# Optimization experiments

Measured on AMD Instinct MI355X. Metric: run time of the kernel, lower is better.

The kernel has to match this reference:

```python
import jax, jax.numpy as jnp
import numpy as np

T, B, C, S = 4096, 8, 512, 2048


def setup_inputs() -> dict:
    key = jax.random.key(0)
    k1, k2, k3 = jax.random.split(key, 3)
    x = jax.random.normal(k1, (T, B, C), dtype=jnp.float32)
    downsampling_mask = jax.random.uniform(k2, (B, T, S), dtype=jnp.float32)
    size_of_groups = jax.random.randint(k3, (B, S), 0, 4, dtype=jnp.int64)
    leftmost_group = jnp.zeros((1, 1, C), dtype=jnp.float32)
    return {"x": x, "downsampling_mask": downsampling_mask,
            "size_of_groups": size_of_groups, "leftmost_group": leftmost_group}


def reference(x, downsampling_mask, size_of_groups, leftmost_group):
    # mode == 'average': masked grouped pooling as a dense contraction
    # x: [T,B,C], mask: [B,T,S] -> downsampled: [S,B,C]
    downsampled = jnp.einsum('tbc,bts->sbc', x, downsampling_mask)
    # prepend learned leftmost group embedding, broadcast over batch
    left = jnp.broadcast_to(leftmost_group, (1, x.shape[1], x.shape[2]))
    return jnp.concatenate([left, downsampled], axis=0)  # [S+1, B, C]
```

## Files before the change

### kernel.cpp

```cpp
#include <hip/hip_runtime.h>
#include <hip/hip_bf16.h>

constexpr int T  = 4096;
constexpr int Bb = 8;
constexpr int C  = 512;
constexpr int S  = 2048;
constexpr int BC = Bb * C;

constexpr int BK = 64;
constexpr int NK = T / BK;

typedef __bf16 bf16x8 __attribute__((ext_vector_type(8)));
typedef float  f32x16 __attribute__((ext_vector_type(16)));
typedef float  f32x4  __attribute__((ext_vector_type(4)));

__device__ inline unsigned pk2(float lo, float hi) {
    union { __hip_bfloat16 h; unsigned short u; } a, b;
    a.h = __float2bfloat16(lo);
    b.h = __float2bfloat16(hi);
    return ((unsigned)b.u << 16) | (unsigned)a.u;
}

__device__ inline int slot16(int s) { return s ^ ((s >> 2) & 7); }

__global__ void left_fill(const float* __restrict__ left, float* __restrict__ out) {
    int i = blockIdx.x * blockDim.x + threadIdx.x;
    if (i < BC) out[i] = left[i & (C - 1)];
}

__global__ __launch_bounds__(512, 4) void ds_gemm(
    const float* __restrict__ x,
    const float* __restrict__ mask,
    float* __restrict__ out)
{
    __shared__ __align__(16) unsigned char smem[65536];

    const int bid0 = blockIdx.x;
    const int xcd  = bid0 & 7;
    const int slot = bid0 >> 3;
    const int b    = xcd;
    const int mt   = slot & 15;
    const int nt   = (slot >> 4) & 3;

    const int tid  = threadIdx.x;
    const int lane = tid & 63;
    const int wave = tid >> 6;
    const int h    = wave >> 2;
    const int wq   = wave & 3;
    const int wm = wq >> 1;
    const int wn = wq & 1;
    const int lm = lane & 31;
    const int kg = lane >> 5;

    const int  ii  = tid & 255;
    const int  sg  = ii & 31;
    const int  tg  = ii >> 5;
    const bool stB = (tid >= 256);

    const float* gsrc = stB
        ? x    + (size_t)(tg * 8) * BC + b * C + nt * 128 + sg * 4
        : mask + (size_t)b * T * S + (size_t)(tg * 8) * S + mt * 128 + sg * 4;
    const size_t grow  = stB ? (size_t)BC : (size_t)S;
    const size_t gstep = grow * BK;

    int waddr[4];
#pragma unroll
    for (int j = 0; j < 4; ++j)
        waddr[j] = (stB ? 16384 : 0) + tg * 2048 + slot16(sg * 4 + j) * 16;

    int raddrA[2][2], raddrB[2][2];
#pragma unroll
    for (int kk = 0; kk < 2; ++kk)
#pragma unroll
        for (int q = 0; q < 2; ++q) {
            const int oct = h * 4 + kk * 2 + kg;
            raddrA[kk][q] = oct * 2048 + slot16(wm * 64 + q * 32 + lm) * 16;
            raddrB[kk][q] = 16384 + oct * 2048 + slot16(wn * 64 + q * 32 + lm) * 16;
        }

    f32x16 acc[2][2] = {};
    f32x4  L[8];

#define LOAD_TILE(k)                                                        \
    {                                                                       \
        const float* p_ = gsrc + (size_t)(k) * gstep;                       \
        _Pragma("unroll") for (int r = 0; r < 8; ++r)                       \
            L[r] = *(const f32x4*)(p_ + (size_t)r * grow);                  \
    }

#define WRITE_TILE(buf)                                                     \
    {                                                                       \
        const int boff_ = (buf) * 32768;                                    \
        _Pragma("unroll") for (int j = 0; j < 4; ++j) {                     \
            uint4 w_;                                                       \
            w_.x = pk2(L[0][j], L[1][j]);                                   \
            w_.y = pk2(L[2][j], L[3][j]);                                   \
            w_.z = pk2(L[4][j], L[5][j]);                                   \
            w_.w = pk2(L[6][j], L[7][j]);                                   \
            *(uint4*)(smem + boff_ + waddr[j]) = w_;                        \
        }                                                                   \
    }

#define COMPUTE(buf)                                                        \
    {                                                                       \
        const int boff_ = (buf) * 32768;                                    \
        _Pragma("unroll") for (int kk = 0; kk < 2; ++kk) {                  \
            bf16x8 a0_ = *(const bf16x8*)(smem + boff_ + raddrA[kk][0]);    \
            bf16x8 a1_ = *(const bf16x8*)(smem + boff_ + raddrA[kk][1]);    \
            bf16x8 b0_ = *(const bf16x8*)(smem + boff_ + raddrB[kk][0]);    \
            bf16x8 b1_ = *(const bf16x8*)(smem + boff_ + raddrB[kk][1]);    \
            acc[0][0] = __builtin_amdgcn_mfma_f32_32x32x16_bf16(a0_, b0_, acc[0][0], 0, 0, 0); \
            acc[0][1] = __builtin_amdgcn_mfma_f32_32x32x16_bf16(a0_, b1_, acc[0][1], 0, 0, 0); \
            acc[1][0] = __builtin_amdgcn_mfma_f32_32x32x16_bf16(a1_, b0_, acc[1][0], 0, 0, 0); \
            acc[1][1] = __builtin_amdgcn_mfma_f32_32x32x16_bf16(a1_, b1_, acc[1][1], 0, 0, 0); \
        }                                                                   \
    }

    LOAD_TILE(0);

    for (int k = 0; k < NK; ++k) {
        WRITE_TILE(k & 1);
        if (k + 1 < NK) LOAD_TILE(k + 1);
        __syncthreads();
        COMPUTE(k & 1);
    }

#undef LOAD_TILE
#undef WRITE_TILE
#undef COMPUTE

    __syncthreads();
    if (h == 1) {
#pragma unroll
        for (int m2 = 0; m2 < 2; ++m2)
#pragma unroll
            for (int n2 = 0; n2 < 2; ++n2) {
                unsigned char* base = smem + (wave - 4) * 16384 + (m2 * 2 + n2) * 4096 + lane * 16;
#pragma unroll
                for (int r4 = 0; r4 < 4; ++r4) {
                    f32x4 v = { acc[m2][n2][r4 * 4 + 0], acc[m2][n2][r4 * 4 + 1],
                                acc[m2][n2][r4 * 4 + 2], acc[m2][n2][r4 * 4 + 3] };
                    *(f32x4*)(base + r4 * 1024) = v;
                }
            }
    }
    __syncthreads();
    if (h == 0) {
#pragma unroll
        for (int m2 = 0; m2 < 2; ++m2)
#pragma unroll
            for (int n2 = 0; n2 < 2; ++n2) {
                const unsigned char* base = smem + wave * 16384 + (m2 * 2 + n2) * 4096 + lane * 16;
#pragma unroll
                for (int r4 = 0; r4 < 4; ++r4) {
                    f32x4 v = *(const f32x4*)(base + r4 * 1024);
#pragma unroll
                    for (int j = 0; j < 4; ++j) acc[m2][n2][r4 * 4 + j] += v[j];
                }
            }

        const int s_w = mt * 128 + wm * 64;
        const int c_w = nt * 128 + wn * 64;
        float* outp = out + BC;
#pragma unroll
        for (int m2 = 0; m2 < 2; ++m2)
#pragma unroll
            for (int n2 = 0; n2 < 2; ++n2)
#pragma unroll
                for (int r = 0; r < 16; ++r) {
                    const int row  = (r & 3) + 8 * (r >> 2) + 4 * kg;
                    const int srow = s_w + m2 * 32 + row;
                    const int ccol = c_w + n2 * 32 + lm;
                    outp[(size_t)srow * BC + b * C + ccol] = acc[m2][n2][r];
                }
    }
}

extern "C" void kernel_launch(void* const* d_in, const int* in_sizes, int n_in,
                              void* d_out, int out_size, void* d_ws, size_t ws_size,
                              hipStream_t stream) {
    const float* x    = (const float*)d_in[0];
    const float* mask = (const float*)d_in[1];
    const float* left = (const float*)d_in[3];
    float* out = (float*)d_out;

    left_fill<<<BC / 256, 256, 0, stream>>>(left, out);
    ds_gemm<<<Bb * (S / 128) * (C / 128), 512, 0, stream>>>(x, mask, out);
}
```

Before: 142.0 us.

## Shrink GEMM tile to 128x64 with 256-thread blocks and K-step 32

Changes the output tile from 128x128 to 128x64, cuts blocks from 512 to 256 threads (4 waves, 2-way K-split), and halves the K-step to 32 with a smaller 24KB double-buffered shared-memory stage. The launch grid doubles, which targets occupancy and load balance across the CUs. The trade-off is that each x/mask element is re-read more times from global memory (mask traffic doubles because of the narrower N tile), and the loop takes more iterations with more syncs per unit of work.

```diff
diff --git a/kernel.cpp b/kernel.cpp
--- a/kernel.cpp
+++ b/kernel.cpp
@@ -7,7 +7,7 @@
 constexpr int S  = 2048;
 constexpr int BC = Bb * C;
 
-constexpr int BK = 64;
+constexpr int BK = 32;
 constexpr int NK = T / BK;
 
 typedef __bf16 bf16x8 __attribute__((ext_vector_type(8)));
@@ -28,69 +28,66 @@
     if (i < BC) out[i] = left[i & (C - 1)];
 }
 
-__global__ __launch_bounds__(512, 4) void ds_gemm(
+__global__ __launch_bounds__(256, 4) void ds_gemm(
     const float* __restrict__ x,
     const float* __restrict__ mask,
     float* __restrict__ out)
 {
-    __shared__ __align__(16) unsigned char smem[65536];
+    __shared__ __align__(16) unsigned char smem[32768];
 
     const int bid0 = blockIdx.x;
     const int xcd  = bid0 & 7;
     const int slot = bid0 >> 3;
     const int b    = xcd;
     const int mt   = slot & 15;
-    const int nt   = (slot >> 4) & 3;
+    const int nt   = slot >> 4;
 
     const int tid  = threadIdx.x;
     const int lane = tid & 63;
     const int wave = tid >> 6;
-    const int h    = wave >> 2;
-    const int wq   = wave & 3;
-    const int wm = wq >> 1;
-    const int wn = wq & 1;
+    const int h    = wave >> 1;
+    const int wm   = wave & 1;
     const int lm = lane & 31;
     const int kg = lane >> 5;
 
-    const int  ii  = tid & 255;
-    const int  sg  = ii & 31;
-    const int  tg  = ii >> 5;
-    const bool stB = (tid >= 256);
+    const bool stA = (tid < 128);
+    const bool stG = (tid < 192);
+    const int  ii  = stA ? tid : (tid - 128);
+    const int  sg  = stA ? (ii & 31) : (ii & 15);
+    const int  tg  = stA ? (ii >> 5) : (ii >> 4);
 
-    const float* gsrc = stB
-        ? x    + (size_t)(tg * 8) * BC + b * C + nt * 128 + sg * 4
-        : mask + (size_t)b * T * S + (size_t)(tg * 8) * S + mt * 128 + sg * 4;
-    const size_t grow  = stB ? (size_t)BC : (size_t)S;
+    const float* gsrc = stA
+        ? mask + (size_t)b * T * S + (size_t)(tg * 8) * S + mt * 128 + sg * 4
+        : x    + (size_t)(tg * 8) * BC + b * C + nt * 64 + sg * 4;
+    const size_t grow  = stA ? (size_t)S : (size_t)BC;
     const size_t gstep = grow * BK;
 
     int waddr[4];
 #pragma unroll
     for (int j = 0; j < 4; ++j)
-        waddr[j] = (stB ? 16384 : 0) + tg * 2048 + slot16(sg * 4 + j) * 16;
+        waddr[j] = stA ? (tg * 2048 + slot16(sg * 4 + j) * 16)
+                       : (8192 + tg * 1024 + slot16(sg * 4 + j) * 16);
 
-    int raddrA[2][2], raddrB[2][2];
+    int raddrA[2], raddrB[2];
 #pragma unroll
-    for (int kk = 0; kk < 2; ++kk)
-#pragma unroll
-        for (int q = 0; q < 2; ++q) {
-            const int oct = h * 4 + kk * 2 + kg;
-            raddrA[kk][q] = oct * 2048 + slot16(wm * 64 + q * 32 + lm) * 16;
-            raddrB[kk][q] = 16384 + oct * 2048 + slot16(wn * 64 + q * 32 + lm) * 16;
-        }
+    for (int q = 0; q < 2; ++q) {
+        raddrA[q] = (h * 2 + kg) * 2048 + slot16(wm * 64 + q * 32 + lm) * 16;
+        raddrB[q] = 8192 + (h * 2 + kg) * 1024 + slot16(q * 32 + lm) * 16;
+    }
 
     f32x16 acc[2][2] = {};
     f32x4  L[8];
 
 #define LOAD_TILE(k)                                                        \
-    {                                                                       \
+    if (stG) {                                                              \
         const float* p_ = gsrc + (size_t)(k) * gstep;                       \
         _Pragma("unroll") for (int r = 0; r < 8; ++r)                       \
             L[r] = *(const f32x4*)(p_ + (size_t)r * grow);                  \
     }
 
 #define WRITE_TILE(buf)                                                     \
-    {                                                                       \
-        const int boff_ = (buf) * 32768;                                    \
+    if (stG) {                                                              \
+        const int boff_ = (buf) * 12288;                                    \
         _Pragma("unroll") for (int j = 0; j < 4; ++j) {                     \
             uint4 w_;                                                       \
             w_.x = pk2(L[0][j], L[1][j]);                                   \
@@ -103,17 +100,15 @@
 
 #define COMPUTE(buf)                                                        \
     {                                                                       \
-        const int boff_ = (buf) * 32768;                                    \
-        _Pragma("unroll") for (int kk = 0; kk < 2; ++kk) {                  \
-            bf16x8 a0_ = *(const bf16x8*)(smem + boff_ + raddrA[kk][0]);    \
-            bf16x8 a1_ = *(const bf16x8*)(smem + boff_ + raddrA[kk][1]);    \
-            bf16x8 b0_ = *(const bf16x8*)(smem + boff_ + raddrB[kk][0]);    \
-            bf16x8 b1_ = *(const bf16x8*)(smem + boff_ + raddrB[kk][1]);    \
-            acc[0][0] = __builtin_amdgcn_mfma_f32_32x32x16_bf16(a0_, b0_, acc[0][0], 0, 0, 0); \
-            acc[0][1] = __builtin_amdgcn_mfma_f32_32x32x16_bf16(a0_, b1_, acc[0][1], 0, 0, 0); \
-            acc[1][0] = __builtin_amdgcn_mfma_f32_32x32x16_bf16(a1_, b0_, acc[1][0], 0, 0, 0); \
-            acc[1][1] = __builtin_amdgcn_mfma_f32_32x32x16_bf16(a1_, b1_, acc[1][1], 0, 0, 0); \
-        }                                                                   \
+        const int boff_ = (buf) * 12288;                                    \
+        bf16x8 a0_ = *(const bf16x8*)(smem + boff_ + raddrA[0]);            \
+        bf16x8 a1_ = *(const bf16x8*)(smem + boff_ + raddrA[1]);            \
+        bf16x8 b0_ = *(const bf16x8*)(smem + boff_ + raddrB[0]);            \
+        bf16x8 b1_ = *(const bf16x8*)(smem + boff_ + raddrB[1]);            \
+        acc[0][0] = __builtin_amdgcn_mfma_f32_32x32x16_bf16(a0_, b0_, acc[0][0], 0, 0, 0); \
+        acc[0][1] = __builtin_amdgcn_mfma_f32_32x32x16_bf16(a0_, b1_, acc[0][1], 0, 0, 0); \
+        acc[1][0] = __builtin_amdgcn_mfma_f32_32x32x16_bf16(a1_, b0_, acc[1][0], 0, 0, 0); \
+        acc[1][1] = __builtin_amdgcn_mfma_f32_32x32x16_bf16(a1_, b1_, acc[1][1], 0, 0, 0); \
     }
 
     LOAD_TILE(0);
@@ -135,7 +130,7 @@
         for (int m2 = 0; m2 < 2; ++m2)
 #pragma unroll
             for (int n2 = 0; n2 < 2; ++n2) {
-                unsigned char* base = smem + (wave - 4) * 16384 + (m2 * 2 + n2) * 4096 + lane * 16;
+                unsigned char* base = smem + (wave - 2) * 16384 + (m2 * 2 + n2) * 4096 + lane * 16;
 #pragma unroll
                 for (int r4 = 0; r4 < 4; ++r4) {
                     f32x4 v = { acc[m2][n2][r4 * 4 + 0], acc[m2][n2][r4 * 4 + 1],
@@ -160,7 +155,7 @@
             }
 
         const int s_w = mt * 128 + wm * 64;
-        const int c_w = nt * 128 + wn * 64;
+        const int c_w = nt * 64;
         float* outp = out + BC;
 #pragma unroll
         for (int m2 = 0; m2 < 2; ++m2)
@@ -185,5 +180,5 @@
     float* out = (float*)d_out;
 
     left_fill<<<BC / 256, 256, 0, stream>>>(left, out);
-    ds_gemm<<<Bb * (S / 128) * (C / 128), 512, 0, stream>>>(x, mask, out);
+    ds_gemm<<<Bb * (S / 128) * (C / 64), 256, 0, stream>>>(x, mask, out);
 }
```

Measured after the change: 329.9 us. 132% more time.

## Pre-transpose x to bf16 and feed B fragments straight from global memory

Applied to the files above, without the earlier changes.

Adds a kernel that transposes x into a [B*C, T] bf16 buffer in workspace. The GEMM kernel then loads B-operand fragments straight from global memory into registers, and only the mask tile is staged through LDS, which halves LDS traffic and LDS use per block. This is meant to cut the B-side LDS write/read and the fp32-to-bf16 conversion inside the GEMM loop. In exchange it adds an extra pass over x plus a kernel launch, and the direct B loads may not be hidden behind compute. The old path is kept as a fallback when the workspace is too small.

```diff
diff --git a/kernel.cpp b/kernel.cpp
--- a/kernel.cpp
+++ b/kernel.cpp
@@ -28,8 +28,40 @@
     if (i < BC) out[i] = left[i & (C - 1)];
 }
 
-__global__ __launch_bounds__(512, 4) void ds_gemm(
-    const float* __restrict__ x,
+__global__ __launch_bounds__(256) void transpose_x(
+    const float* __restrict__ x, __bf16* __restrict__ xT)
+{
+    __shared__ float lds[64][68];
+    const int bid = blockIdx.x;
+    const int b   = bid >> 9;
+    const int rem = bid & 511;
+    const int t0  = (rem >> 3) * 64;
+    const int c0  = (rem & 7) * 64;
+    const int tid = threadIdx.x;
+
+#pragma unroll
+    for (int it = 0; it < 4; ++it) {
+        const int slot = tid + it * 256;
+        const int row = slot >> 4, cg = slot & 15;
+        f32x4 v = *(const f32x4*)(x + (size_t)(t0 + row) * BC + b * C + c0 + cg * 4);
+        *(f32x4*)(&lds[row][cg * 4]) = v;
+    }
+    __syncthreads();
+#pragma unroll
+    for (int it = 0; it < 2; ++it) {
+        const int slot = tid + it * 256;
+        const int cr = slot >> 3, tg8 = slot & 7;
+        uint4 w;
+        w.x = pk2(lds[tg8 * 8 + 0][cr], lds[tg8 * 8 + 1][cr]);
+        w.y = pk2(lds[tg8 * 8 + 2][cr], lds[tg8 * 8 + 3][cr]);
+        w.z = pk2(lds[tg8 * 8 + 4][cr], lds[tg8 * 8 + 5][cr]);
+        w.w = pk2(lds[tg8 * 8 + 6][cr], lds[tg8 * 8 + 7][cr]);
+        *(uint4*)(xT + (size_t)(b * C + c0 + cr) * T + t0 + tg8 * 8) = w;
+    }
+}
+
+__global__ __launch_bounds__(512, 4) void ds_gemm_direct(
+    const __bf16* __restrict__ xT,
     const float* __restrict__ mask,
     float* __restrict__ out)
 {
@@ -52,22 +84,152 @@
     const int lm = lane & 31;
     const int kg = lane >> 5;
 
-    const int  ii  = tid & 255;
-    const int  sg  = ii & 31;
-    const int  tg  = ii >> 5;
+    const int sg = tid & 31;
+    const int tq = tid >> 5;
+
+    const float* gsrc = mask + (size_t)b * T * S + (size_t)(tq * 4) * S + mt * 128 + sg * 4;
+    const size_t gstep = (size_t)S * BK;
+
+    int waddr[4];
+#pragma unroll
+    for (int j = 0; j < 4; ++j)
+        waddr[j] = (tq >> 1) * 2048 + slot16(sg * 4 + j) * 16 + (tq & 1) * 8;
+
+    int raddrA[2][2];
+#pragma unroll
+    for (int kk = 0; kk < 2; ++kk)
+#pragma unroll
+        for (int q = 0; q < 2; ++q)
+            raddrA[kk][q] = (h * 4 + kk * 2 + kg) * 2048 + slot16(wm * 64 + q * 32 + lm) * 16;
+
+    const __bf16* colptr[2];
+#pragma unroll
+    for (int n2 = 0; n2 < 2; ++n2)
+        colptr[n2] = xT + (size_t)(b * C + nt * 128 + wn * 64 + n2 * 32 + lm) * T
+                        + (h * 4 + kg) * 8;
+
+    f32x16 acc[2][2] = {};
+    f32x4  L[4];
+    bf16x8 Bf[2][2];
+
+#define LOAD_A(k)                                                           \
+    {                                                                       \
+        const float* p_ = gsrc + (size_t)(k) * gstep;                       \
+        _Pragma("unroll") for (int r = 0; r < 4; ++r)                       \
+            L[r] = *(const f32x4*)(p_ + (size_t)r * S);                     \
+    }
+
+#define WRITE_A(buf)                                                        \
+    {                                                                       \
+        const int boff_ = (buf) * 16384;                                    \
+        _Pragma("unroll") for (int j = 0; j < 4; ++j) {                     \
+            uint2 w_;                                                       \
+            w_.x = pk2(L[0][j], L[1][j]);                                   \
+            w_.y = pk2(L[2][j], L[3][j]);                                   \
+            *(uint2*)(smem + boff_ + waddr[j]) = w_;                        \
+        }                                                                   \
+    }
+
+#define LOAD_B(k)                                                           \
+    {                                                                       \
+        _Pragma("unroll") for (int kk = 0; kk < 2; ++kk)                    \
+        _Pragma("unroll") for (int n2 = 0; n2 < 2; ++n2)                    \
+            Bf[kk][n2] = *(const bf16x8*)(colptr[n2] + (size_t)(k) * 64 + kk * 16); \
+    }
+
+#define COMPUTE(buf)                                                        \
+    {                                                                       \
+        const int boff_ = (buf) * 16384;                                    \
+        _Pragma("unroll") for (int kk = 0; kk < 2; ++kk) {                  \
+            bf16x8 a0_ = *(const bf16x8*)(smem + boff_ + raddrA[kk][0]);    \
+            bf16x8 a1_ = *(const bf16x8*)(smem + boff_ + raddrA[kk][1]);    \
+            acc[0][0] = __builtin_amdgcn_mfma_f32_32x32x16_bf16(a0_, Bf[kk][0], acc[0][0], 0, 0, 0); \
+            acc[0][1] = __builtin_amdgcn_mfma_f32_32x32x16_bf16(a0_, Bf[kk][1], acc[0][1], 0, 0, 0); \
+            acc[1][0] = __builtin_amdgcn_mfma_f32_32x32x16_bf16(a1_, Bf[kk][0], acc[1][0], 0, 0, 0); \
+            acc[1][1] = __builtin_amdgcn_mfma_f32_32x32x16_bf16(a1_, Bf[kk][1], acc[1][1], 0, 0, 0); \
+        }                                                                   \
+    }
+
+    LOAD_A(0);
+    for (int k = 0; k < NK; ++k) {
+        LOAD_B(k);
+        WRITE_A(k & 1);
+        if (k + 1 < NK) LOAD_A(k + 1);
+        __syncthreads();
+        COMPUTE(k & 1);
+    }
+
+#undef LOAD_A
+#undef WRITE_A
+#undef LOAD_B
+#undef COMPUTE
+
+    __syncthreads();
+    if (h == 1) {
+#pragma unroll
+        for (int m2 = 0; m2 < 2; ++m2)
+#pragma unroll
+            for (int n2 = 0; n2 < 2; ++n2) {
+                unsigned char* base = smem + (wave - 4) * 16384 + (m2 * 2 + n2) * 4096 + lane * 16;
+#pragma unroll
+                for (int r4 = 0; r4 < 4; ++r4) {
+                    f32x4 v = { acc[m2][n2][r4 * 4 + 0], acc[m2][n2][r4 * 4 + 1],
+                                acc[m2][n2][r4 * 4 + 2], acc[m2][n2][r4 * 4 + 3] };
+                    *(f32x4*)(base + r4 * 1024) = v;
+                }
+            }
+    }
+    __syncthreads();
+    if (h == 0) {
+#pragma unroll
+        for (int m2 = 0; m2 < 2; ++m2)
+#pragma unroll
+            for (int n2 = 0; n2 < 2; ++n2) {
+                const unsigned char* base = smem + wave * 16384 + (m2 * 2 + n2) * 4096 + lane * 16;
+#pragma unroll
+                for (int r4 = 0; r4 < 4; ++r4) {
+                    f32x4 v = *(const f32x4*)(base + r4 * 1024);
+#pragma unroll
+                    for (int j = 0; j < 4; ++j) acc[m2][n2][r4 * 4 + j] += v[j];
+                }
+            }
+        const int s_w = mt * 128 + wm * 64;
+        const int c_w = nt * 128 + wn * 64;
+        float* outp = out + BC;
+#pragma unroll
+        for (int m2 = 0; m2 < 2; ++m2)
+#pragma unroll
+            for (int n2 = 0; n2 < 2; ++n2)
+#pragma unroll
+                for (int r = 0; r < 16; ++r) {
+                    const int row  = (r & 3) + 8 * (r >> 2) + 4 * kg;
+                    outp[(size_t)(s_w + m2 * 32 + row) * BC + b * C + c_w + n2 * 32 + lm]
+                        = acc[m2][n2][r];
+                }
+    }
+}
+
+__global__ __launch_bounds__(512, 4) void ds_gemm_fb(
+    const float* __restrict__ x, const float* __restrict__ mask, float* __restrict__ out)
+{
+    __shared__ __align__(16) unsigned char smem[65536];
+    const int bid0 = blockIdx.x;
+    const int xcd = bid0 & 7, slot = bid0 >> 3;
+    const int b = xcd, mt = slot & 15, nt = (slot >> 4) & 3;
+    const int tid = threadIdx.x, lane = tid & 63, wave = tid >> 6;
+    const int h = wave >> 2, wq = wave & 3, wm = wq >> 1, wn = wq & 1;
+    const int lm = lane & 31, kg = lane >> 5;
+    const int ii = tid & 255, sg = ii & 31, tg = ii >> 5;
     const bool stB = (tid >= 256);
-
     const float* gsrc = stB
         ? x    + (size_t)(tg * 8) * BC + b * C + nt * 128 + sg * 4
         : mask + (size_t)b * T * S + (size_t)(tg * 8) * S + mt * 128 + sg * 4;
-    const size_t grow  = stB ? (size_t)BC : (size_t)S;
+    const size_t grow = stB ? (size_t)BC : (size_t)S;
     const size_t gstep = grow * BK;
-
     int waddr[4];
 #pragma unroll
     for (int j = 0; j < 4; ++j)
         waddr[j] = (stB ? 16384 : 0) + tg * 2048 + slot16(sg * 4 + j) * 16;
-
     int raddrA[2][2], raddrB[2][2];
 #pragma unroll
     for (int kk = 0; kk < 2; ++kk)
@@ -77,58 +239,35 @@
             raddrA[kk][q] = oct * 2048 + slot16(wm * 64 + q * 32 + lm) * 16;
             raddrB[kk][q] = 16384 + oct * 2048 + slot16(wn * 64 + q * 32 + lm) * 16;
         }
-
     f32x16 acc[2][2] = {};
-    f32x4  L[8];
-
-#define LOAD_TILE(k)                                                        \
-    {                                                                       \
-        const float* p_ = gsrc + (size_t)(k) * gstep;                       \
-        _Pragma("unroll") for (int r = 0; r < 8; ++r)                       \
-            L[r] = *(const f32x4*)(p_ + (size_t)r * grow);                  \
-    }
-
-#define WRITE_TILE(buf)                                                     \
-    {                                                                       \
-        const int boff_ = (buf) * 32768;                                    \
-        _Pragma("unroll") for (int j = 0; j < 4; ++j) {                     \
-            uint4 w_;                                                       \
-            w_.x = pk2(L[0][j], L[1][j]);                                   \
-            w_.y = pk2(L[2][j], L[3][j]);                                   \
-            w_.z = pk2(L[4][j], L[5][j]);                                   \
-            w_.w = pk2(L[6][j], L[7][j]);                                   \
-            *(uint4*)(smem + boff_ + waddr[j]) = w_;                        \
-        }                                                                   \
-    }
-
-#define COMPUTE(buf)                                                        \
-    {                                                                       \
-        const int boff_ = (buf) * 32768;                                    \
-        _Pragma("unroll") for (int kk = 0; kk < 2; ++kk) {                  \
-            bf16x8 a0_ = *(const bf16x8*)(smem + boff_ + raddrA[kk][0]);    \
-            bf16x8 a1_ = *(const bf16x8*)(smem + boff_ + raddrA[kk][1]);    \
-            bf16x8 b0_ = *(const bf16x8*)(smem + boff_ + raddrB[kk][0]);    \
-            bf16x8 b1_ = *(const bf16x8*)(smem + boff_ + raddrB[kk][1]);    \
-            acc[0][0] = __builtin_amdgcn_mfma_f32_32x32x16_bf16(a0_, b0_, acc[0][0], 0, 0, 0); \
-            acc[0][1] = __builtin_amdgcn_mfma_f32_32x32x16_bf16(a0_, b1_, acc[0][1], 0, 0, 0); \
-            acc[1][0] = __builtin_amdgcn_mfma_f32_32x32x16_bf16(a1_, b0_, acc[1][0], 0, 0, 0); \
-            acc[1][1] = __builtin_amdgcn_mfma_f32_32x32x16_bf16(a1_, b1_, acc[1][1], 0, 0, 0); \
-        }                                                                   \
-    }
-
+    f32x4 L[8];
+#define LOAD_TILE(k) { const float* p_ = gsrc + (size_t)(k) * gstep; \
+    _Pragma("unroll") for (int r = 0; r < 8; ++r) L[r] = *(const f32x4*)(p_ + (size_t)r * grow); }
+#define WRITE_TILE(buf) { const int boff_ = (buf) * 32768; \
+    _Pragma("unroll") for (int j = 0; j < 4; ++j) { uint4 w_; \
+        w_.x = pk2(L[0][j], L[1][j]); w_.y = pk2(L[2][j], L[3][j]); \
+        w_.z = pk2(L[4][j], L[5][j]); w_.w = pk2(L[6][j], L[7][j]); \
+        *(uint4*)(smem + boff_ + waddr[j]) = w_; } }
+#define COMPUTE(buf) { const int boff_ = (buf) * 32768; \
+    _Pragma("unroll") for (int kk = 0; kk < 2; ++kk) { \
+        bf16x8 a0_ = *(const bf16x8*)(smem + boff_ + raddrA[kk][0]); \
+        bf16x8 a1_ = *(const bf16x8*)(smem + boff_ + raddrA[kk][1]); \
+        bf16x8 b0_ = *(const bf16x8*)(smem + boff_ + raddrB[kk][0]); \
+        bf16x8 b1_ = *(const bf16x8*)(smem + boff_ + raddrB[kk][1]); \
+        acc[0][0] = __builtin_amdgcn_mfma_f32_32x32x16_bf16(a0_, b0_, acc[0][0], 0, 0, 0); \
+        acc[0][1] = __builtin_amdgcn_mfma_f32_32x32x16_bf16(a0_, b1_, acc[0][1], 0, 0, 0); \
+        acc[1][0] = __builtin_amdgcn_mfma_f32_32x32x16_bf16(a1_, b0_, acc[1][0], 0, 0, 0); \
+        acc[1][1] = __builtin_amdgcn_mfma_f32_32x32x16_bf16(a1_, b1_, acc[1][1], 0, 0, 0); } }
     LOAD_TILE(0);
-
     for (int k = 0; k < NK; ++k) {
         WRITE_TILE(k & 1);
         if (k + 1 < NK) LOAD_TILE(k + 1);
         __syncthreads();
         COMPUTE(k & 1);
     }
-
 #undef LOAD_TILE
 #undef WRITE_TILE
 #undef COMPUTE
-
     __syncthreads();
     if (h == 1) {
 #pragma unroll
@@ -158,7 +297,6 @@
                     for (int j = 0; j < 4; ++j) acc[m2][n2][r4 * 4 + j] += v[j];
                 }
             }
-
         const int s_w = mt * 128 + wm * 64;
         const int c_w = nt * 128 + wn * 64;
         float* outp = out + BC;
@@ -168,10 +306,9 @@
             for (int n2 = 0; n2 < 2; ++n2)
 #pragma unroll
                 for (int r = 0; r < 16; ++r) {
-                    const int row  = (r & 3) + 8 * (r >> 2) + 4 * kg;
-                    const int srow = s_w + m2 * 32 + row;
-                    const int ccol = c_w + n2 * 32 + lm;
-                    outp[(size_t)srow * BC + b * C + ccol] = acc[m2][n2][r];
+                    const int row = (r & 3) + 8 * (r >> 2) + 4 * kg;
+                    outp[(size_t)(s_w + m2 * 32 + row) * BC + b * C + c_w + n2 * 32 + lm]
+                        = acc[m2][n2][r];
                 }
     }
 }
@@ -185,5 +322,13 @@
     float* out = (float*)d_out;
 
     left_fill<<<BC / 256, 256, 0, stream>>>(left, out);
-    ds_gemm<<<Bb * (S / 128) * (C / 128), 512, 0, stream>>>(x, mask, out);
-}
+
+    const size_t XT_BYTES = (size_t)T * Bb * C * sizeof(__bf16);
+    if (ws_size >= XT_BYTES) {
+        __bf16* xT = (__bf16*)d_ws;
+        transpose_x<<<Bb * (T / 64) * (C / 64), 256, 0, stream>>>(x, xT);
+        ds_gemm_direct<<<Bb * (S / 128) * (C / 128), 512, 0, stream>>>(xT, mask, out);
+    } else {
+        ds_gemm_fb<<<Bb * (S / 128) * (C / 128), 512, 0, stream>>>(x, mask, out);
+    }
+}
```

After: 216.7 us. 1.53x slower.
